# Kernel tuning notes

Hardware: AMD Instinct MI355X
Metric: run time of the kernel (lower is better)

The kernel has to match this reference:

```python
import jax, jax.numpy as jnp
import numpy as np
import math

N, S, T, D = 4, 2048, 2048, 1024

def setup_inputs() -> dict:
    key = jax.random.key(0)
    ks = jax.random.split(key, 6)
    scale = 1.0 / math.sqrt(D)
    return {
        "query": jax.random.normal(ks[0], (N, S, D), dtype=jnp.float32),
        "key": jax.random.normal(ks[1], (N, T, D), dtype=jnp.float32),
        "value": jax.random.normal(ks[2], (N, T, D), dtype=jnp.float32),
        # causal mask: 1 = attend, 0 = masked out (masked_fill where mask == 0)
        "attn_mask": jnp.tril(jnp.ones((S, T), dtype=jnp.int32)),
        "Wq": jax.random.normal(ks[3], (D, D), dtype=jnp.float32) * scale,
        "Wk": jax.random.normal(ks[4], (D, D), dtype=jnp.float32) * scale,
        "Wv": jax.random.normal(ks[5], (D, D), dtype=jnp.float32) * scale,
    }

def reference(query, key, value, attn_mask, Wq, Wk, Wv):
    # nn.Linear(bias=False): y = x @ W.T
    q = jnp.einsum('nsd,ed->nse', query, Wq)
    k = jnp.einsum('ntd,ed->nte', key, Wk)
    v = jnp.einsum('ntd,ed->nte', value, Wv)
    # scaled dot-product scores [N, S, T]
    dot = jnp.einsum('nse,nte->nst', q, k) / jnp.sqrt(jnp.asarray(D, q.dtype))
    dot = jnp.where(attn_mask == 0, -jnp.inf, dot)
    scores = jax.nn.softmax(dot, axis=-1)
    # dropout is identity in eval mode
    y = jnp.einsum('nst,nte->nse', scores, v)
    return y
```

## Files before the change

kernel.cpp:

```cpp
#include <hip/hip_runtime.h>
#include <math.h>

using u16 = unsigned short;
typedef __attribute__((ext_vector_type(8))) __bf16 bf16x8;
typedef __attribute__((ext_vector_type(4))) float f32x4;
typedef __attribute__((ext_vector_type(4))) float f4v;
typedef __attribute__((ext_vector_type(8))) u16 u16x8;

__device__ __forceinline__ u16 f2bf(float f) {
  unsigned u = __float_as_uint(f);
  u += 0x7fffu + ((u >> 16) & 1u);
  return (u16)(u >> 16);
}
__device__ __forceinline__ float bf2f(u16 b) {
  unsigned u = ((unsigned)b) << 16;
  return __uint_as_float(u);
}

__device__ __forceinline__ void gload16(const void* g, void* l) {
  __builtin_amdgcn_global_load_lds(
      (const __attribute__((address_space(1))) unsigned int*)g,
      (__attribute__((address_space(3))) unsigned int*)l, 16, 0, 0);
}

__device__ __forceinline__ f32x4 MF(bf16x8 a, bf16x8 b, f32x4 c) {
  return __builtin_amdgcn_mfma_f32_16x16x32_bf16(a, b, c, 0, 0, 0);
}

__global__ __launch_bounds__(256) void cast3_f32_bf16(
    const float* __restrict__ p0, const float* __restrict__ p1,
    const float* __restrict__ p2, u16* __restrict__ out, size_t ostride) {
  int z = blockIdx.z;
  const float* in = (z == 0) ? p0 : (z == 1) ? p1 : p2;
  size_t i = ((size_t)blockIdx.x * 256 + threadIdx.x) * 8;
  f4v a = *reinterpret_cast<const f4v*>(in + i);
  f4v b = *reinterpret_cast<const f4v*>(in + i + 4);
  u16x8 r;
  r[0] = f2bf(a[0]); r[1] = f2bf(a[1]); r[2] = f2bf(a[2]); r[3] = f2bf(a[3]);
  r[4] = f2bf(b[0]); r[5] = f2bf(b[1]); r[6] = f2bf(b[2]); r[7] = f2bf(b[3]);
  *reinterpret_cast<u16x8*>(out + z * ostride + i) = r;
}

__global__ __launch_bounds__(256) void tcast_w(
    const float* __restrict__ wk, const float* __restrict__ wq,
    u16* __restrict__ wkT, u16* __restrict__ wqT) {
  __shared__ float t[64][65];
  int z = blockIdx.z;
  const float* I = z ? wq : wk;
  u16* O = z ? wqT : wkT;
  int c0 = blockIdx.x * 64, r0 = blockIdx.y * 64;
  int tx = threadIdx.x & 63, ty = threadIdx.x >> 6;
  #pragma unroll
  for (int i = 0; i < 64; i += 4)
    t[ty + i][tx] = I[(size_t)(r0 + ty + i) * 1024 + c0 + tx];
  __syncthreads();
  #pragma unroll
  for (int i = 0; i < 64; i += 4)
    O[(size_t)(c0 + ty + i) * 1024 + r0 + tx] = f2bf(t[tx][ty + i]);
}

__global__ __launch_bounds__(256) void transpose_bf16k(const u16* __restrict__ in,
                                                       u16* __restrict__ out) {
  __shared__ u16 t[64][65];
  int c0 = blockIdx.x * 64, r0 = blockIdx.y * 64;
  size_t zb = (size_t)blockIdx.z * 2048 * 1024;
  const u16* I = in + zb;
  u16* O = out + zb;
  int tx = threadIdx.x & 63, ty = threadIdx.x >> 6;
  #pragma unroll
  for (int i = 0; i < 64; i += 4)
    t[ty + i][tx] = I[(size_t)(r0 + ty + i) * 1024 + c0 + tx];
  __syncthreads();
  #pragma unroll
  for (int i = 0; i < 64; i += 4)
    O[(size_t)(c0 + ty + i) * 2048 + r0 + tx] = t[tx][ty + i];
}

template<typename OutT, int MODE>
__global__ __launch_bounds__(512) void gemm_bt8(
    const u16* __restrict__ A, const u16* __restrict__ B, OutT* __restrict__ C,
    int K, int lda, int ldb, int ldc,
    size_t sA, size_t sB, size_t sC, float alpha,
    OutT* __restrict__ C1) {
  int bn, bm, bz = 0;
  int kEnd = K;
  const u16 *Ag, *Bg;
  OutT* Cg;
  if (MODE == 0) {
    bm = blockIdx.x >> 3;
    bn = blockIdx.x & 7;
    Ag = A + (size_t)bm * 128 * lda;
    Bg = B + (size_t)bn * 128 * ldb;
    Cg = C;
  } else if (MODE == 1) {
    int h = blockIdx.x;
    int l = (h & 7) * 68 + (h >> 3);
    bz = l / 136;
    int t = l % 136;
    bm = (int)((sqrtf(8.f * (float)t + 1.f) - 1.f) * 0.5f);
    while ((bm + 1) * (bm + 2) / 2 <= t) ++bm;
    while (bm * (bm + 1) / 2 > t) --bm;
    bn = t - bm * (bm + 1) / 2;
    Ag = A + sA * bz + (size_t)bm * 128 * lda;
    Bg = B + sB * bz + (size_t)bn * 128 * ldb;
    Cg = C + sC * bz;
  } else if (MODE == 2) {
    int l = blockIdx.x;
    bm = 15 - (l >> 5);
    int rest = l & 31;
    bz = rest >> 3;
    bn = rest & 7;
    kEnd = (K < (bm + 1) * 128) ? K : (bm + 1) * 128;
    Ag = A + sA * bz + (size_t)bm * 128 * lda;
    Bg = B + sB * bz + (size_t)bn * 128 * ldb;
    Cg = C + sC * bz;
  } else {
    int h = blockIdx.x;
    int l = (h & 7) * 128 + (h >> 3);
    bn = l & 7;
    int bm128 = l >> 3;
    int which = bm128 >> 6;
    bm = bm128 & 63;
    Ag = A + (size_t)bm128 * 128 * lda;
    Bg = B + (size_t)which * sB + (size_t)bn * 128 * ldb;
    Cg = (which == 0) ? C : C1;
  }

  __shared__ __align__(16) u16 As[2][128 * 32];
  __shared__ __align__(16) u16 Bs[2][128 * 32];

  const int tid = threadIdx.x;
  const int lane = tid & 63, wv = tid >> 6;
  const int wr = wv >> 2, wc = wv & 3;
  const int fr = lane & 15, kq = (lane >> 4) * 8;

  const int e0 = wv * 512 + lane * 8;
  const int r0 = e0 >> 5, c0 = e0 & 31;
  const u16* a0 = Ag + (size_t)r0 * lda + c0;
  const u16* b0 = Bg + (size_t)r0 * ldb + c0;

  f32x4 acc[4][2] = {};
  const int nt = kEnd / 32;

  gload16(a0, &As[0][wv * 512]);
  gload16(b0, &Bs[0][wv * 512]);
  __syncthreads();

  for (int t = 0; t < nt; ++t) {
    const int cur = t & 1;
    if (t + 1 < nt) {
      const int k0 = (t + 1) * 32;
      gload16(a0 + k0, &As[cur ^ 1][wv * 512]);
      gload16(b0 + k0, &Bs[cur ^ 1][wv * 512]);
    }
    bf16x8 af[4], bfv[2];
    #pragma unroll
    for (int m = 0; m < 4; ++m)
      af[m] = *reinterpret_cast<const bf16x8*>(&As[cur][(wr * 64 + m * 16 + fr) * 32 + kq]);
    #pragma unroll
    for (int n = 0; n < 2; ++n)
      bfv[n] = *reinterpret_cast<const bf16x8*>(&Bs[cur][(wc * 32 + n * 16 + fr) * 32 + kq]);
    #pragma unroll
    for (int m = 0; m < 4; ++m)
      #pragma unroll
      for (int n = 0; n < 2; ++n)
        acc[m][n] = MF(af[m], bfv[n], acc[m][n]);
    __syncthreads();
  }

  const int row0 = bm * 128 + wr * 64 + (lane >> 4) * 4;
  const int col0 = bn * 128 + wc * 32 + fr;
  #pragma unroll
  for (int m = 0; m < 4; ++m)
    #pragma unroll
    for (int n = 0; n < 2; ++n) {
      #pragma unroll
      for (int j = 0; j < 4; ++j) {
        float val = acc[m][n][j] * alpha;
        size_t idx = (size_t)(row0 + m * 16 + j) * ldc + (col0 + n * 16);
        if constexpr (sizeof(OutT) == 2) Cg[idx] = f2bf(val);
        else Cg[idx] = val;
      }
    }
}

__global__ __launch_bounds__(256) void softmax_causal(u16* __restrict__ sc) {
  int r = blockIdx.x;
  int s = r & 2047;
  u16* row = sc + (size_t)r * 2048;
  int tid = threadIdx.x;
  int t0 = tid * 8;
  u16x8 raw = {0, 0, 0, 0, 0, 0, 0, 0};
  if (t0 <= s) raw = *reinterpret_cast<const u16x8*>(row + t0);
  float v[8];
  float mx = -1e30f;
  #pragma unroll
  for (int j = 0; j < 8; ++j) {
    v[j] = ((t0 + j) <= s) ? bf2f(raw[j]) : -1e30f;
    mx = fmaxf(mx, v[j]);
  }
  #pragma unroll
  for (int o = 32; o; o >>= 1) mx = fmaxf(mx, __shfl_xor(mx, o, 64));
  __shared__ float red[8];
  if ((tid & 63) == 0) red[tid >> 6] = mx;
  __syncthreads();
  mx = fmaxf(fmaxf(red[0], red[1]), fmaxf(red[2], red[3]));
  float p[8];
  float sum = 0.f;
  #pragma unroll
  for (int j = 0; j < 8; ++j) {
    p[j] = ((t0 + j) <= s) ? __expf(v[j] - mx) : 0.f;
    sum += p[j];
  }
  #pragma unroll
  for (int o = 32; o; o >>= 1) sum += __shfl_xor(sum, o, 64);
  if ((tid & 63) == 0) red[4 + (tid >> 6)] = sum;
  __syncthreads();
  sum = red[4] + red[5] + red[6] + red[7];
  float inv = 1.0f / sum;
  u16x8 o8;
  #pragma unroll
  for (int j = 0; j < 8; ++j) o8[j] = f2bf(p[j] * inv);
  if (t0 <= (s | 127))
    *reinterpret_cast<u16x8*>(row + t0) = o8;
}

extern "C" void kernel_launch(void* const* d_in, const int* in_sizes, int n_in,
                              void* d_out, int out_size, void* d_ws, size_t ws_size,
                              hipStream_t stream) {
  const float* q  = (const float*)d_in[0];
  const float* k  = (const float*)d_in[1];
  const float* v  = (const float*)d_in[2];
  const float* Wq = (const float*)d_in[4];
  const float* Wk = (const float*)d_in[5];
  const float* Wv = (const float*)d_in[6];
  float* out = (float*)d_out;
  char* ws = (char*)d_ws;

  const size_t MB = 1024ull * 1024ull;
  u16* sc   = (u16*)ws;
  u16* qb   = (u16*)ws;
  u16* xk   = (u16*)(ws + 32 * MB);
  u16* wsl  = (u16*)(ws + 48 * MB);
  u16* wkT  = (u16*)(ws + 52 * MB);
  u16* wqT  = (u16*)(ws + 54 * MB);
  u16* Vp   = (u16*)(ws + 56 * MB);
  u16* Vt   = (u16*)(ws + 72 * MB);
  u16* Yq   = (u16*)(ws + 88 * MB);
  (void)in_sizes; (void)n_in; (void)out_size; (void)ws_size;

  cast3_f32_bf16<<<dim3(4096, 1, 3), 256, 0, stream>>>(q, v, k, qb, 8ull * MB);

  tcast_w<<<dim3(16, 16, 2), 256, 0, stream>>>(Wk, Wq, wkT, wqT);
  cast3_f32_bf16<<<dim3(512, 1, 1), 256, 0, stream>>>(Wv, nullptr, nullptr,
                                                      wsl + 1048576, 0);

  gemm_bt8<u16, 0><<<64, 512, 0, stream>>>(
      wkT, wqT, wsl, 1024, 1024, 1024, 1024, 0, 0, 0, 1.0f, nullptr);

  gemm_bt8<u16, 3><<<1024, 512, 0, stream>>>(
      qb, wsl, Yq, 1024, 1024, 1024, 1024,
      0, 1ull * MB, 0, 1.0f, Vp);

  transpose_bf16k<<<dim3(16, 32, 4), 256, 0, stream>>>(Vp, Vt);

  gemm_bt8<u16, 1><<<544, 512, 0, stream>>>(
      Yq, xk, sc, 1024, 1024, 1024, 2048,
      (size_t)2048 * 1024, (size_t)2048 * 1024, (size_t)2048 * 2048, 0.03125f,
      nullptr);

  softmax_causal<<<8192, 256, 0, stream>>>(sc);

  gemm_bt8<float, 2><<<512, 512, 0, stream>>>(
      sc, Vt, out, 2048, 2048, 2048, 1024,
      (size_t)2048 * 2048, (size_t)1024 * 2048, (size_t)2048 * 1024, 1.0f,
      nullptr);
}
```

Measured before the change: 179.0 us.

## Fuse V transpose into projection GEMM epilogue and merge weight prep kernels

The V-projection blocks of the mode-3 GEMM now transpose their output tile through shared memory and write directly into the transposed V layout. This removes the separate transpose kernel and the intermediate Vp buffer round-trip. The Wk/Wq transpose-cast and the Wv cast are merged into one launch, and the input cast is reordered after the weight GEMM. This saves launches and memory traffic, at the cost of a larger shared allocation and an extra barrier in the epilogue.

```diff
diff --git a/kernel.cpp b/kernel.cpp
--- a/kernel.cpp
+++ b/kernel.cpp
@@ -41,39 +41,37 @@
   *reinterpret_cast<u16x8*>(out + z * ostride + i) = r;
 }
 
-__global__ __launch_bounds__(256) void tcast_w(
-    const float* __restrict__ wk, const float* __restrict__ wq,
-    u16* __restrict__ wkT, u16* __restrict__ wqT) {
-  __shared__ float t[64][65];
+__global__ __launch_bounds__(256) void wprep(
+    const float* __restrict__ Wk, const float* __restrict__ Wq,
+    const float* __restrict__ Wv, u16* __restrict__ wkT,
+    u16* __restrict__ wqT, u16* __restrict__ wv_bf) {
   int z = blockIdx.z;
-  const float* I = z ? wq : wk;
-  u16* O = z ? wqT : wkT;
-  int c0 = blockIdx.x * 64, r0 = blockIdx.y * 64;
-  int tx = threadIdx.x & 63, ty = threadIdx.x >> 6;
-  #pragma unroll
-  for (int i = 0; i < 64; i += 4)
-    t[ty + i][tx] = I[(size_t)(r0 + ty + i) * 1024 + c0 + tx];
-  __syncthreads();
-  #pragma unroll
-  for (int i = 0; i < 64; i += 4)
-    O[(size_t)(c0 + ty + i) * 1024 + r0 + tx] = f2bf(t[tx][ty + i]);
-}
-
-__global__ __launch_bounds__(256) void transpose_bf16k(const u16* __restrict__ in,
-                                                       u16* __restrict__ out) {
-  __shared__ u16 t[64][65];
-  int c0 = blockIdx.x * 64, r0 = blockIdx.y * 64;
-  size_t zb = (size_t)blockIdx.z * 2048 * 1024;
-  const u16* I = in + zb;
-  u16* O = out + zb;
-  int tx = threadIdx.x & 63, ty = threadIdx.x >> 6;
-  #pragma unroll
-  for (int i = 0; i < 64; i += 4)
-    t[ty + i][tx] = I[(size_t)(r0 + ty + i) * 1024 + c0 + tx];
-  __syncthreads();
-  #pragma unroll
-  for (int i = 0; i < 64; i += 4)
-    O[(size_t)(c0 + ty + i) * 2048 + r0 + tx] = t[tx][ty + i];
+  if (z < 2) {
+    __shared__ float t[64][65];
+    const float* I = z ? Wq : Wk;
+    u16* O = z ? wqT : wkT;
+    int c0 = blockIdx.x * 64, r0 = blockIdx.y * 64;
+    int tx = threadIdx.x & 63, ty = threadIdx.x >> 6;
+    #pragma unroll
+    for (int i = 0; i < 64; i += 4)
+      t[ty + i][tx] = I[(size_t)(r0 + ty + i) * 1024 + c0 + tx];
+    __syncthreads();
+    #pragma unroll
+    for (int i = 0; i < 64; i += 4)
+      O[(size_t)(c0 + ty + i) * 1024 + r0 + tx] = f2bf(t[tx][ty + i]);
+  } else {
+    int b = blockIdx.y * 16 + blockIdx.x;
+    size_t i = (size_t)b * 4096 + threadIdx.x * 16;
+    #pragma unroll
+    for (int h = 0; h < 2; ++h) {
+      f4v a = *reinterpret_cast<const f4v*>(Wv + i + h * 8);
+      f4v c = *reinterpret_cast<const f4v*>(Wv + i + h * 8 + 4);
+      u16x8 r;
+      r[0] = f2bf(a[0]); r[1] = f2bf(a[1]); r[2] = f2bf(a[2]); r[3] = f2bf(a[3]);
+      r[4] = f2bf(c[0]); r[5] = f2bf(c[1]); r[6] = f2bf(c[2]); r[7] = f2bf(c[3]);
+      *reinterpret_cast<u16x8*>(wv_bf + i + h * 8) = r;
+    }
+  }
 }
 
 template<typename OutT, int MODE>
@@ -84,6 +82,7 @@
     OutT* __restrict__ C1) {
   int bn, bm, bz = 0;
   int kEnd = K;
+  bool whichV = false;
   const u16 *Ag, *Bg;
   OutT* Cg;
   if (MODE == 0) {
@@ -119,15 +118,16 @@
     int l = (h & 7) * 128 + (h >> 3);
     bn = l & 7;
     int bm128 = l >> 3;
-    int which = bm128 >> 6;
+    whichV = (bm128 >> 6) != 0;
     bm = bm128 & 63;
     Ag = A + (size_t)bm128 * 128 * lda;
-    Bg = B + (size_t)which * sB + (size_t)bn * 128 * ldb;
-    Cg = (which == 0) ? C : C1;
-  }
-
-  __shared__ __align__(16) u16 As[2][128 * 32];
-  __shared__ __align__(16) u16 Bs[2][128 * 32];
+    Bg = B + (whichV ? sB : 0) + (size_t)bn * 128 * ldb;
+    Cg = C;
+  }
+
+  __shared__ __align__(16) char smem[33024];
+  u16* AsB = (u16*)smem;
+  u16* BsB = AsB + 8192;
 
   const int tid = threadIdx.x;
   const int lane = tid & 63, wv = tid >> 6;
@@ -142,30 +142,59 @@
   f32x4 acc[4][2] = {};
   const int nt = kEnd / 32;
 
-  gload16(a0, &As[0][wv * 512]);
-  gload16(b0, &Bs[0][wv * 512]);
+  gload16(a0, &AsB[wv * 512]);
+  gload16(b0, &BsB[wv * 512]);
   __syncthreads();
 
   for (int t = 0; t < nt; ++t) {
     const int cur = t & 1;
     if (t + 1 < nt) {
       const int k0 = (t + 1) * 32;
-      gload16(a0 + k0, &As[cur ^ 1][wv * 512]);
-      gload16(b0 + k0, &Bs[cur ^ 1][wv * 512]);
+      gload16(a0 + k0, &AsB[(cur ^ 1) * 4096 + wv * 512]);
+      gload16(b0 + k0, &BsB[(cur ^ 1) * 4096 + wv * 512]);
     }
+    const u16* Ac = AsB + cur * 4096;
+    const u16* Bc = BsB + cur * 4096;
     bf16x8 af[4], bfv[2];
     #pragma unroll
     for (int m = 0; m < 4; ++m)
-      af[m] = *reinterpret_cast<const bf16x8*>(&As[cur][(wr * 64 + m * 16 + fr) * 32 + kq]);
+      af[m] = *reinterpret_cast<const bf16x8*>(&Ac[(wr * 64 + m * 16 + fr) * 32 + kq]);
     #pragma unroll
     for (int n = 0; n < 2; ++n)
-      bfv[n] = *reinterpret_cast<const bf16x8*>(&Bs[cur][(wc * 32 + n * 16 + fr) * 32 + kq]);
+      bfv[n] = *reinterpret_cast<const bf16x8*>(&Bc[(wc * 32 + n * 16 + fr) * 32 + kq]);
     #pragma unroll
     for (int m = 0; m < 4; ++m)
       #pragma unroll
       for (int n = 0; n < 2; ++n)
         acc[m][n] = MF(af[m], bfv[n], acc[m][n]);
     __syncthreads();
+  }
+
+  if constexpr (MODE == 3) {
+    if (whichV) {
+      u16* tt = (u16*)smem;
+      #pragma unroll
+      for (int m = 0; m < 4; ++m)
+        #pragma unroll
+        for (int n = 0; n < 2; ++n)
+          #pragma unroll
+          for (int j = 0; j < 4; ++j)
+            tt[(wr * 64 + (lane >> 4) * 4 + m * 16 + j) * 129 +
+               (wc * 32 + fr + n * 16)] = f2bf(acc[m][n][j]);
+      __syncthreads();
+      const int orow = tid >> 2, oc = (tid & 3) * 32;
+      size_t base = (size_t)(bm >> 4) * (1024 * 2048) +
+                    (size_t)(bn * 128 + orow) * 2048 +
+                    (size_t)(bm & 15) * 128 + oc;
+      #pragma unroll
+      for (int jj = 0; jj < 4; ++jj) {
+        u16x8 o;
+        #pragma unroll
+        for (int j = 0; j < 8; ++j) o[j] = tt[(oc + jj * 8 + j) * 129 + orow];
+        *reinterpret_cast<u16x8*>(&C1[base + jj * 8]) = o;
+      }
+      return;
+    }
   }
 
   const int row0 = bm * 128 + wr * 64 + (lane >> 4) * 4;
@@ -244,25 +273,21 @@
   u16* wsl  = (u16*)(ws + 48 * MB);
   u16* wkT  = (u16*)(ws + 52 * MB);
   u16* wqT  = (u16*)(ws + 54 * MB);
-  u16* Vp   = (u16*)(ws + 56 * MB);
-  u16* Vt   = (u16*)(ws + 72 * MB);
-  u16* Yq   = (u16*)(ws + 88 * MB);
+  u16* Vt   = (u16*)(ws + 56 * MB);
+  u16* Yq   = (u16*)(ws + 72 * MB);
   (void)in_sizes; (void)n_in; (void)out_size; (void)ws_size;
 
-  cast3_f32_bf16<<<dim3(4096, 1, 3), 256, 0, stream>>>(q, v, k, qb, 8ull * MB);
-
-  tcast_w<<<dim3(16, 16, 2), 256, 0, stream>>>(Wk, Wq, wkT, wqT);
-  cast3_f32_bf16<<<dim3(512, 1, 1), 256, 0, stream>>>(Wv, nullptr, nullptr,
-                                                      wsl + 1048576, 0);
+  wprep<<<dim3(16, 16, 3), 256, 0, stream>>>(Wk, Wq, Wv, wkT, wqT,
+                                             wsl + 1048576);
 
   gemm_bt8<u16, 0><<<64, 512, 0, stream>>>(
       wkT, wqT, wsl, 1024, 1024, 1024, 1024, 0, 0, 0, 1.0f, nullptr);
 
+  cast3_f32_bf16<<<dim3(4096, 1, 3), 256, 0, stream>>>(q, v, k, qb, 8ull * MB);
+
   gemm_bt8<u16, 3><<<1024, 512, 0, stream>>>(
       qb, wsl, Yq, 1024, 1024, 1024, 1024,
-      0, 1ull * MB, 0, 1.0f, Vp);
-
-  transpose_bf16k<<<dim3(16, 32, 4), 256, 0, stream>>>(Vp, Vt);
+      0, 1048576, 0, 1.0f, Vt);
 
   gemm_bt8<u16, 1><<<544, 512, 0, stream>>>(
       Yq, xk, sc, 1024, 1024, 1024, 2048,
```

New measurement: 170.8 us. 4.6% less time.
